# Kernel tuning notes

Hardware: AMD Instinct MI355X
Metric: run time of the kernel (lower is better)

## Reference

```python
import jax, jax.numpy as jnp
import numpy as np

B, T, I, H = 32, 512, 512, 1024


def setup_inputs() -> dict:
    key = jax.random.key(0)
    ks = jax.random.split(key, 9)
    k = 1.0 / np.sqrt(H)  # torch nn.RNN init: U(-1/sqrt(H), 1/sqrt(H))
    u = lambda kk, sh: jax.random.uniform(kk, sh, jnp.float32, -k, k)
    return {
        "x": jax.random.normal(ks[0], (B, T, I), jnp.float32),
        "W_ih0": u(ks[1], (H, I)),
        "W_hh0": u(ks[2], (H, H)),
        "b_ih0": u(ks[3], (H,)),
        "b_hh0": u(ks[4], (H,)),
        "W_ih1": u(ks[5], (H, H)),
        "W_hh1": u(ks[6], (H, H)),
        "b_ih1": u(ks[7], (H,)),
        "b_hh1": u(ks[8], (H,)),
    }


def _rnn_layer(x_tbi, Wih, Whh, bih, bhh):
    # Precompute input projection for all timesteps: [T, B, H]
    xw = jnp.einsum('tbi,hi->tbh', x_tbi, Wih) + bih + bhh
    h0 = jnp.zeros((x_tbi.shape[1], Whh.shape[0]), x_tbi.dtype)

    def step(h, xw_t):
        h = jnp.tanh(xw_t + h @ Whh.T)
        return h, h

    _, hs = jax.lax.scan(step, h0, xw)
    return hs  # [T, B, H]


def reference(x, W_ih0, W_hh0, b_ih0, b_hh0, W_ih1, W_hh1, b_ih1, b_hh1):
    x_tbi = jnp.transpose(x, (1, 0, 2))  # [T, B, I]
    h1 = _rnn_layer(x_tbi, W_ih0, W_hh0, b_ih0, b_hh0)
    h2 = _rnn_layer(h1, W_ih1, W_hh1, b_ih1, b_hh1)
    return jnp.transpose(h2, (1, 0, 2))  # [B, T, H]
```

## Files before the change

### kernel.cpp

```cpp
#include <hip/hip_runtime.h>
#include <hip/hip_bf16.h>


#define B_ 32
#define T_ 512
#define I_ 512
#define H_ 1024

typedef __attribute__((ext_vector_type(8))) short short8;
typedef __attribute__((ext_vector_type(4))) float float4v;

#define OFF_XBF   0ull
#define OFF_H1    16777216ull
#define OFF_HPING 50397184ull
#define OFF_FLAGS 50528256ull

#define WAIT_VM0() asm volatile("s_waitcnt vmcnt(0)" ::: "memory")
#define CFENCE()   asm volatile("" ::: "memory")

#define LDF(f, base, O) \
  asm volatile("global_load_dwordx4 %0, %1, off offset:%2 sc1" \
               : "=v"(f) : "v"(base), "n"(O) : "memory")

#define LD8(F, S, BASE, OB) \
  LDF(F[S+0], BASE, OB+0);   LDF(F[S+1], BASE, OB+64); \
  LDF(F[S+2], BASE, OB+128); LDF(F[S+3], BASE, OB+192); \
  LDF(F[S+4], BASE, OB+256); LDF(F[S+5], BASE, OB+320); \
  LDF(F[S+6], BASE, OB+384); LDF(F[S+7], BASE, OB+448)

#define VMW8(N, F, S) \
  asm volatile("s_waitcnt vmcnt(" #N ")" \
               : "+v"(F[S+0]), "+v"(F[S+1]), "+v"(F[S+2]), "+v"(F[S+3]), \
                 "+v"(F[S+4]), "+v"(F[S+5]), "+v"(F[S+6]), "+v"(F[S+7]))

#define MFMA_B(acc, f, kb) \
  acc = __builtin_amdgcn_mfma_f32_16x16x32_bf16( \
      f, *reinterpret_cast<const short8*>(ldsW + (kb) * 512 + lofs), acc, 0, 0, 0)

#define MF8(F, S, KB) \
  MFMA_B(accA, F[S+0], KB+0); MFMA_B(accB, F[S+1], KB+1); \
  MFMA_B(accA, F[S+2], KB+2); MFMA_B(accB, F[S+3], KB+3); \
  MFMA_B(accA, F[S+4], KB+4); MFMA_B(accB, F[S+5], KB+5); \
  MFMA_B(accA, F[S+6], KB+6); MFMA_B(accB, F[S+7], KB+7)

__device__ __forceinline__ float fast_tanh(float x) {
  float z = fminf(2.885390081777927f * x, 60.0f);
  float e = __builtin_amdgcn_exp2f(z);
  return 1.0f - 2.0f * __builtin_amdgcn_rcpf(e + 1.0f);
}

__device__ __forceinline__ void wait_layer(unsigned* fbase, int lane, int wid, unsigned s) {
  unsigned* p = fbase + (((unsigned)lane << 1) + wid) * 16;
  while (__hip_atomic_load(p, __ATOMIC_RELAXED, __HIP_MEMORY_SCOPE_AGENT) < s)
    __builtin_amdgcn_s_sleep(1);
  CFENCE();
}

__global__ __launch_bounds__(128)
void rnn_fused(const float* __restrict__ Wih0, const float* __restrict__ Whh0,
               const float* __restrict__ bih0, const float* __restrict__ bhh0,
               const float* __restrict__ Wih1, const float* __restrict__ Whh1,
               const float* __restrict__ bih1, const float* __restrict__ bhh1,
               const __hip_bfloat16* __restrict__ x_bf,
               __hip_bfloat16* __restrict__ h1buf,
               __hip_bfloat16* __restrict__ hping,
               float* __restrict__ out,
               unsigned* __restrict__ flags)
{
  __shared__ unsigned short ldsW[16 * 2048];
  const int tid  = threadIdx.x;
  const int wgid = blockIdx.x;
  const bool isL1 = (wgid >= 64);
  const int wg   = isL1 ? wgid - 64 : wgid;
  const int KIN  = isL1 ? H_ : I_;
  const int KTOT = KIN + H_;
  const float* Wih = isL1 ? Wih1 : Wih0;
  const float* Whh = isL1 ? Whh1 : Whh0;

  for (int idx = tid; idx < 16 * KTOT; idx += 128) {
    int c = idx / KTOT;
    int k = idx - c * KTOT;
    float w = (k < KIN) ? Wih[(size_t)(wg * 16 + c) * KIN + k]
                        : Whh[(size_t)(wg * 16 + c) * H_ + (k - KIN)];
    __hip_bfloat16 hb = __float2bfloat16(w);
    int pos = ((k >> 5) * 64 + ((k >> 3) & 3) * 16 + c) * 8 + (k & 7);
    ldsW[pos] = *reinterpret_cast<unsigned short*>(&hb);
  }

  const int lane  = tid & 63;
  const int wid   = tid >> 6;
  const int col   = wg * 16 + (lane & 15);
  const float biasv = isL1 ? (bih1[col] + bhh1[col]) : (bih0[col] + bhh0[col]);
  const int arow  = wid * 16 + (lane & 15);
  const int ksub  = ((lane >> 4) & 3) * 8;
  const int lofs  = lane * 8;
  const int rbase = wid * 16 + (lane >> 4) * 4;
  const int r0    = (lane & 1) ? 2 : 0;
  const int colp  = col & ~1;

  unsigned* fl0 = flags;
  unsigned* fl1 = flags + 128 * 16;
  unsigned* myflag = (isL1 ? fl1 : fl0) + (((unsigned)wg << 1) + wid) * 16;

  __syncthreads();

  if (!isL1) {
    for (int s = 0; s < T_; ++s) {
      float4v accA = {biasv, biasv, biasv, biasv};
      float4v accB = {0.f, 0.f, 0.f, 0.f};
      const __hip_bfloat16* a0 = x_bf + (size_t)arow * (T_ * I_) + (size_t)s * I_ + ksub;
#pragma unroll
      for (int kb = 0; kb < 16; ++kb) {
        short8 av = *reinterpret_cast<const short8*>(a0 + kb * 32);
        MFMA_B(accA, av, kb);
      }
      if (s > 0) wait_layer(fl0, lane, wid, (unsigned)s);
      const __hip_bfloat16* a1 = h1buf + (size_t)s * (B_ * H_) + (size_t)arow * H_ + ksub;
      short8 g[32];
      LD8(g, 0, a1, 0);  LD8(g, 8, a1, 512);  LD8(g, 16, a1, 1024);  LD8(g, 24, a1, 1536);
      VMW8(24, g, 0);   MF8(g, 0, 16);
      VMW8(16, g, 8);   MF8(g, 8, 24);
      VMW8(8,  g, 16);  MF8(g, 16, 32);
      VMW8(0,  g, 24);  MF8(g, 24, 40);

      __hip_bfloat16* hd = h1buf + (size_t)(s + 1) * (B_ * H_);
      float hv[4];
#pragma unroll
      for (int r = 0; r < 4; ++r) hv[r] = fast_tanh(accA[r] + accB[r]);
#pragma unroll
      for (int r = 0; r < 4; ++r) {
        float other = __shfl_xor(hv[r], 1, 64);
        float lo = (lane & 1) ? other : hv[r];
        float hi = (lane & 1) ? hv[r] : other;
        if (r == r0 || r == r0 + 1) {
          __hip_bfloat16 l16 = __float2bfloat16(lo), h16 = __float2bfloat16(hi);
          unsigned pk = (unsigned)*(unsigned short*)&l16 | ((unsigned)*(unsigned short*)&h16 << 16);
          unsigned* dst = (unsigned*)(hd + (size_t)(rbase + r) * H_ + colp);
          __hip_atomic_store(dst, pk, __ATOMIC_RELAXED, __HIP_MEMORY_SCOPE_AGENT);
        }
      }
      WAIT_VM0();
      if (lane == 0)
        __hip_atomic_store(myflag, (unsigned)(s + 1), __ATOMIC_RELAXED, __HIP_MEMORY_SCOPE_AGENT);
    }
  } else {
    for (int t = 0; t < T_; ++t) {
      float4v accA = {biasv, biasv, biasv, biasv};
      float4v accB = {0.f, 0.f, 0.f, 0.f};
      wait_layer(fl0, lane, wid, (unsigned)(t + 1));
      if (t > 0) wait_layer(fl1, lane, wid, (unsigned)t);
      const __hip_bfloat16* aA = h1buf + (size_t)(t + 1) * (B_ * H_) + (size_t)arow * H_ + ksub;
      const __hip_bfloat16* aB = hping + (size_t)(t & 1) * (B_ * H_) + (size_t)arow * H_ + ksub;
      short8 g[32], h[32];
      LD8(g, 0, aA, 0);  LD8(g, 8, aA, 512);  LD8(g, 16, aA, 1024);  LD8(g, 24, aA, 1536);
      VMW8(24, g, 0);   MF8(g, 0, 0);    LD8(h, 0, aB, 0);
      VMW8(24, g, 8);   MF8(g, 8, 8);    LD8(h, 8, aB, 512);
      VMW8(24, g, 16);  MF8(g, 16, 16);  LD8(h, 16, aB, 1024);
      VMW8(24, g, 24);  MF8(g, 24, 24);  LD8(h, 24, aB, 1536);
      VMW8(24, h, 0);   MF8(h, 0, 32);
      VMW8(16, h, 8);   MF8(h, 8, 40);
      VMW8(8,  h, 16);  MF8(h, 16, 48);
      VMW8(0,  h, 24);  MF8(h, 24, 56);

      __hip_bfloat16* hd = hping + (size_t)((t + 1) & 1) * (B_ * H_);
      float hv[4];
#pragma unroll
      for (int r = 0; r < 4; ++r) hv[r] = fast_tanh(accA[r] + accB[r]);
      float lov[4], hiv[4];
#pragma unroll
      for (int r = 0; r < 4; ++r) {
        float other = __shfl_xor(hv[r], 1, 64);
        lov[r] = (lane & 1) ? other : hv[r];
        hiv[r] = (lane & 1) ? hv[r] : other;
        if (r == r0 || r == r0 + 1) {
          __hip_bfloat16 l16 = __float2bfloat16(lov[r]), h16 = __float2bfloat16(hiv[r]);
          unsigned pk = (unsigned)*(unsigned short*)&l16 | ((unsigned)*(unsigned short*)&h16 << 16);
          unsigned* dst = (unsigned*)(hd + (size_t)(rbase + r) * H_ + colp);
          __hip_atomic_store(dst, pk, __ATOMIC_RELAXED, __HIP_MEMORY_SCOPE_AGENT);
        }
      }
      WAIT_VM0();
      if (lane == 0)
        __hip_atomic_store(myflag, (unsigned)(t + 1), __ATOMIC_RELAXED, __HIP_MEMORY_SCOPE_AGENT);
#pragma unroll
      for (int r = 0; r < 4; ++r) {
        if (r == r0 || r == r0 + 1) {
          float2 f2; f2.x = lov[r]; f2.y = hiv[r];
          *(float2*)(out + (size_t)(rbase + r) * (T_ * H_) + (size_t)t * H_ + colp) = f2;
        }
      }
    }
  }
}

__global__ void prep_kernel(const float* __restrict__ x, unsigned long long* __restrict__ x64,
                            unsigned* __restrict__ h1z, unsigned* __restrict__ hpz,
                            unsigned* __restrict__ flags)
{
  int i = blockIdx.x * 256 + threadIdx.x;
  if (i < (B_ * T_ * I_) / 4) {
    const float4* x4 = (const float4*)x;
    float4 v = x4[i];
    __hip_bfloat16 b0 = __float2bfloat16(v.x), b1 = __float2bfloat16(v.y);
    __hip_bfloat16 b2 = __float2bfloat16(v.z), b3 = __float2bfloat16(v.w);
    unsigned long long r = (unsigned long long)*(unsigned short*)&b0
                         | ((unsigned long long)*(unsigned short*)&b1 << 16)
                         | ((unsigned long long)*(unsigned short*)&b2 << 32)
                         | ((unsigned long long)*(unsigned short*)&b3 << 48);
    x64[i] = r;
  }
  if (i < 16384) __hip_atomic_store(h1z + i, 0u, __ATOMIC_RELAXED, __HIP_MEMORY_SCOPE_AGENT);
  if (i < 32768) __hip_atomic_store(hpz + i, 0u, __ATOMIC_RELAXED, __HIP_MEMORY_SCOPE_AGENT);
  if (i < 4096)  __hip_atomic_store(flags + i, 0u, __ATOMIC_RELAXED, __HIP_MEMORY_SCOPE_AGENT);
}

extern "C" void kernel_launch(void* const* d_in, const int* in_sizes, int n_in,
                              void* d_out, int out_size, void* d_ws, size_t ws_size,
                              hipStream_t stream)
{
  const float* x    = (const float*)d_in[0];
  const float* Wih0 = (const float*)d_in[1];
  const float* Whh0 = (const float*)d_in[2];
  const float* bih0 = (const float*)d_in[3];
  const float* bhh0 = (const float*)d_in[4];
  const float* Wih1 = (const float*)d_in[5];
  const float* Whh1 = (const float*)d_in[6];
  const float* bih1 = (const float*)d_in[7];
  const float* bhh1 = (const float*)d_in[8];
  float* out = (float*)d_out;
  char* ws = (char*)d_ws;

  __hip_bfloat16* x_bf  = (__hip_bfloat16*)(ws + OFF_XBF);
  __hip_bfloat16* h1buf = (__hip_bfloat16*)(ws + OFF_H1);
  __hip_bfloat16* hping = (__hip_bfloat16*)(ws + OFF_HPING);
  unsigned* flags = (unsigned*)(ws + OFF_FLAGS);

  prep_kernel<<<(B_ * T_ * I_ / 4 + 255) / 256, 256, 0, stream>>>(
      x, (unsigned long long*)x_bf, (unsigned*)h1buf, (unsigned*)hping, flags);

  rnn_fused<<<128, 128, 0, stream>>>(Wih0, Whh0, bih0, bhh0,
                                     Wih1, Whh1, bih1, bhh1,
                                     x_bf, h1buf, hping, out, flags);
}
```

Measured before the change: 2.844 ms.

## Replace inline-asm sc1 loads and waits with fences and plain loads

Drops the hand-written global_load sc1 asm and staged vmcnt waits in favour of plain loads plus agent-scope acquire/release fences, and turns the hidden-state stores into plain stores. Layer 1 now caches the last observed layer-0 flag value so it skips re-polling when layer 0 is already ahead. The fences may invalidate or write back caches more heavily than the old per-load sc1 bits, and the compiler now controls load/MFMA interleaving, which may lose the hand-tuned overlap.

```diff
diff --git a/kernel.cpp b/kernel.cpp
--- a/kernel.cpp
+++ b/kernel.cpp
@@ -15,33 +15,12 @@
 #define OFF_HPING 50397184ull
 #define OFF_FLAGS 50528256ull
 
-#define WAIT_VM0() asm volatile("s_waitcnt vmcnt(0)" ::: "memory")
-#define CFENCE()   asm volatile("" ::: "memory")
-
-#define LDF(f, base, O) \
-  asm volatile("global_load_dwordx4 %0, %1, off offset:%2 sc1" \
-               : "=v"(f) : "v"(base), "n"(O) : "memory")
-
-#define LD8(F, S, BASE, OB) \
-  LDF(F[S+0], BASE, OB+0);   LDF(F[S+1], BASE, OB+64); \
-  LDF(F[S+2], BASE, OB+128); LDF(F[S+3], BASE, OB+192); \
-  LDF(F[S+4], BASE, OB+256); LDF(F[S+5], BASE, OB+320); \
-  LDF(F[S+6], BASE, OB+384); LDF(F[S+7], BASE, OB+448)
-
-#define VMW8(N, F, S) \
-  asm volatile("s_waitcnt vmcnt(" #N ")" \
-               : "+v"(F[S+0]), "+v"(F[S+1]), "+v"(F[S+2]), "+v"(F[S+3]), \
-                 "+v"(F[S+4]), "+v"(F[S+5]), "+v"(F[S+6]), "+v"(F[S+7]))
+#define FENCE_REL() __builtin_amdgcn_fence(__ATOMIC_RELEASE, "agent")
+#define FENCE_ACQ() __builtin_amdgcn_fence(__ATOMIC_ACQUIRE, "agent")
 
 #define MFMA_B(acc, f, kb) \
   acc = __builtin_amdgcn_mfma_f32_16x16x32_bf16( \
       f, *reinterpret_cast<const short8*>(ldsW + (kb) * 512 + lofs), acc, 0, 0, 0)
-
-#define MF8(F, S, KB) \
-  MFMA_B(accA, F[S+0], KB+0); MFMA_B(accB, F[S+1], KB+1); \
-  MFMA_B(accA, F[S+2], KB+2); MFMA_B(accB, F[S+3], KB+3); \
-  MFMA_B(accA, F[S+4], KB+4); MFMA_B(accB, F[S+5], KB+5); \
-  MFMA_B(accA, F[S+6], KB+6); MFMA_B(accB, F[S+7], KB+7)
 
 __device__ __forceinline__ float fast_tanh(float x) {
   float z = fminf(2.885390081777927f * x, 60.0f);
@@ -49,11 +28,10 @@
   return 1.0f - 2.0f * __builtin_amdgcn_rcpf(e + 1.0f);
 }
 
-__device__ __forceinline__ void wait_layer(unsigned* fbase, int lane, int wid, unsigned s) {
-  unsigned* p = fbase + (((unsigned)lane << 1) + wid) * 16;
+__device__ __forceinline__ void wait_flags(const unsigned* fbase, int lane, int wid, unsigned s) {
+  const unsigned* p = fbase + (((unsigned)lane << 1) + wid) * 16;
   while (__hip_atomic_load(p, __ATOMIC_RELAXED, __HIP_MEMORY_SCOPE_AGENT) < s)
     __builtin_amdgcn_s_sleep(1);
-  CFENCE();
 }
 
 __global__ __launch_bounds__(128)
@@ -114,14 +92,18 @@
         short8 av = *reinterpret_cast<const short8*>(a0 + kb * 32);
         MFMA_B(accA, av, kb);
       }
-      if (s > 0) wait_layer(fl0, lane, wid, (unsigned)s);
+      if (s > 0) wait_flags(fl0, lane, wid, (unsigned)s);
+      FENCE_ACQ();
       const __hip_bfloat16* a1 = h1buf + (size_t)s * (B_ * H_) + (size_t)arow * H_ + ksub;
       short8 g[32];
-      LD8(g, 0, a1, 0);  LD8(g, 8, a1, 512);  LD8(g, 16, a1, 1024);  LD8(g, 24, a1, 1536);
-      VMW8(24, g, 0);   MF8(g, 0, 16);
-      VMW8(16, g, 8);   MF8(g, 8, 24);
-      VMW8(8,  g, 16);  MF8(g, 16, 32);
-      VMW8(0,  g, 24);  MF8(g, 24, 40);
+#pragma unroll
+      for (int kb = 0; kb < 32; ++kb)
+        g[kb] = *reinterpret_cast<const short8*>(a1 + kb * 32);
+#pragma unroll
+      for (int kb = 0; kb < 32; ++kb) {
+        if ((kb & 1) == 0) { MFMA_B(accA, g[kb], 16 + kb); }
+        else               { MFMA_B(accB, g[kb], 16 + kb); }
+      }
 
       __hip_bfloat16* hd = h1buf + (size_t)(s + 1) * (B_ * H_);
       float hv[4];
@@ -135,32 +117,46 @@
         if (r == r0 || r == r0 + 1) {
           __hip_bfloat16 l16 = __float2bfloat16(lo), h16 = __float2bfloat16(hi);
           unsigned pk = (unsigned)*(unsigned short*)&l16 | ((unsigned)*(unsigned short*)&h16 << 16);
-          unsigned* dst = (unsigned*)(hd + (size_t)(rbase + r) * H_ + colp);
-          __hip_atomic_store(dst, pk, __ATOMIC_RELAXED, __HIP_MEMORY_SCOPE_AGENT);
+          *(unsigned*)(hd + (size_t)(rbase + r) * H_ + colp) = pk;
         }
       }
-      WAIT_VM0();
+      FENCE_REL();
       if (lane == 0)
         __hip_atomic_store(myflag, (unsigned)(s + 1), __ATOMIC_RELAXED, __HIP_MEMORY_SCOPE_AGENT);
     }
   } else {
+    const unsigned* shp = fl0 + (((unsigned)lane << 1) + wid) * 16;
+    unsigned sh = 0;
     for (int t = 0; t < T_; ++t) {
       float4v accA = {biasv, biasv, biasv, biasv};
       float4v accB = {0.f, 0.f, 0.f, 0.f};
-      wait_layer(fl0, lane, wid, (unsigned)(t + 1));
-      if (t > 0) wait_layer(fl1, lane, wid, (unsigned)t);
+      unsigned need = (unsigned)(t + 1);
+      while (sh < need) {
+        sh = __hip_atomic_load(shp, __ATOMIC_RELAXED, __HIP_MEMORY_SCOPE_AGENT);
+        if (sh < need) __builtin_amdgcn_s_sleep(1);
+      }
+      if (t > 0) wait_flags(fl1, lane, wid, (unsigned)t);
+      FENCE_ACQ();
       const __hip_bfloat16* aA = h1buf + (size_t)(t + 1) * (B_ * H_) + (size_t)arow * H_ + ksub;
+      short8 g[32];
+#pragma unroll
+      for (int kb = 0; kb < 32; ++kb)
+        g[kb] = *reinterpret_cast<const short8*>(aA + kb * 32);
+#pragma unroll
+      for (int kb = 0; kb < 32; ++kb) {
+        if ((kb & 1) == 0) { MFMA_B(accA, g[kb], kb); }
+        else               { MFMA_B(accB, g[kb], kb); }
+      }
       const __hip_bfloat16* aB = hping + (size_t)(t & 1) * (B_ * H_) + (size_t)arow * H_ + ksub;
-      short8 g[32], h[32];
-      LD8(g, 0, aA, 0);  LD8(g, 8, aA, 512);  LD8(g, 16, aA, 1024);  LD8(g, 24, aA, 1536);
-      VMW8(24, g, 0);   MF8(g, 0, 0);    LD8(h, 0, aB, 0);
-      VMW8(24, g, 8);   MF8(g, 8, 8);    LD8(h, 8, aB, 512);
-      VMW8(24, g, 16);  MF8(g, 16, 16);  LD8(h, 16, aB, 1024);
-      VMW8(24, g, 24);  MF8(g, 24, 24);  LD8(h, 24, aB, 1536);
-      VMW8(24, h, 0);   MF8(h, 0, 32);
-      VMW8(16, h, 8);   MF8(h, 8, 40);
-      VMW8(8,  h, 16);  MF8(h, 16, 48);
-      VMW8(0,  h, 24);  MF8(h, 24, 56);
+      short8 h[32];
+#pragma unroll
+      for (int kb = 0; kb < 32; ++kb)
+        h[kb] = *reinterpret_cast<const short8*>(aB + kb * 32);
+#pragma unroll
+      for (int kb = 0; kb < 32; ++kb) {
+        if ((kb & 1) == 0) { MFMA_B(accA, h[kb], 32 + kb); }
+        else               { MFMA_B(accB, h[kb], 32 + kb); }
+      }
 
       __hip_bfloat16* hd = hping + (size_t)((t + 1) & 1) * (B_ * H_);
       float hv[4];
@@ -175,11 +171,10 @@
         if (r == r0 || r == r0 + 1) {
           __hip_bfloat16 l16 = __float2bfloat16(lov[r]), h16 = __float2bfloat16(hiv[r]);
           unsigned pk = (unsigned)*(unsigned short*)&l16 | ((unsigned)*(unsigned short*)&h16 << 16);
-          unsigned* dst = (unsigned*)(hd + (size_t)(rbase + r) * H_ + colp);
-          __hip_atomic_store(dst, pk, __ATOMIC_RELAXED, __HIP_MEMORY_SCOPE_AGENT);
+          *(unsigned*)(hd + (size_t)(rbase + r) * H_ + colp) = pk;
         }
       }
-      WAIT_VM0();
+      FENCE_REL();
       if (lane == 0)
         __hip_atomic_store(myflag, (unsigned)(t + 1), __ATOMIC_RELAXED, __HIP_MEMORY_SCOPE_AGENT);
 #pragma unroll
```

Result: slower. 6.361 ms (+123.6%).
